# Optimization experiments

Measured on AMD Instinct MI355X. Metric: run time of the kernel, lower is better.

Reference implementation:

```python
import jax, jax.numpy as jnp
import numpy as np

B, V, K, D, E, NE = 32, 512, 16, 128, 32, 8192


def setup_inputs() -> dict:
    key = jax.random.key(0)
    ks = jax.random.split(key, 12)
    s = 0.05
    return {
        "vertex_features": jax.random.normal(ks[0], (B, V, D), jnp.float32),
        "atom_adj": jax.random.randint(ks[1], (B * V * K,), 0, B * V),
        "bond_adj": jax.random.randint(ks[2], (B * V * K,), 0, B * NE),
        "h0": jax.random.normal(ks[3], (B, V, D), jnp.float32),
        "lamda": jnp.full((1,), 0.5, jnp.float32),
        "alpha": jnp.full((1,), 0.1, jnp.float32),
        "l": 1,
        "edge_initial": jax.random.normal(ks[4], (B, NE, E), jnp.float32),
        "vertex_mask": jnp.ones((B, V), jnp.float32),
        "nbs_mask": jax.random.uniform(ks[5], (B, V, K), jnp.float32),
        # label_U1: (D+E) -> D ; label_U2: 2D -> D ; feature_updating: D -> D (variant=False)
        "W1": jax.random.normal(ks[6], (D, D + E), jnp.float32) * s,
        "b1": jax.random.normal(ks[7], (D,), jnp.float32) * s,
        "W2": jax.random.normal(ks[8], (D, 2 * D), jnp.float32) * s,
        "b2": jax.random.normal(ks[9], (D,), jnp.float32) * s,
        "W3": jax.random.normal(ks[10], (D, D), jnp.float32) * s,
        "b3": jax.random.normal(ks[11], (D,), jnp.float32) * s,
    }


def reference(vertex_features, atom_adj, bond_adj, h0, lamda, alpha, l,
              edge_initial, vertex_mask, nbs_mask, W1, b1, W2, b2, W3, b3):
    b, v = vertex_mask.shape
    k = nbs_mask.shape[2]
    d = vertex_features.shape[-1]
    e = edge_initial.shape[-1]
    # gather neighbor vertex and edge features (flat index, torch.index_select semantics)
    vn = vertex_features.reshape(-1, d)[atom_adj].reshape(b, v, k, d)
    en = edge_initial.reshape(-1, e)[bond_adj].reshape(b, v, k, e)
    l_neighbor = jnp.concatenate([vn, en], axis=-1)            # [b,v,k,d+e]
    nl = jax.nn.gelu(l_neighbor @ W1.T + b1, approximate=False)  # exact GELU like torch F.gelu
    nl = jnp.sum(nl * nbs_mask[..., None], axis=-2)            # masked sum over neighbors -> [b,v,d]
    hi = jnp.concatenate([nl, vertex_features], axis=-1) @ W2.T + b2
    theta = jnp.log(lamda / l + 1.0)                           # broadcast scalar (shape [1])
    support = (1.0 - alpha) * hi + alpha * h0                  # variant=False: r == support
    out = theta * (support @ W3.T + b3) + (1.0 - theta) * support
    out = out + vertex_features                                # residual=True
    return out
```

## Files before the change

### kernel.cpp

```cpp
#include <hip/hip_runtime.h>
#include <hip/hip_bf16.h>
#include <math.h>

#define NLSTR 136

typedef __bf16 bf16x8 __attribute__((ext_vector_type(8)));
typedef float f32x4 __attribute__((ext_vector_type(4)));
typedef unsigned short ushort8v __attribute__((ext_vector_type(8)));

union FragU { ushort8v u; bf16x8 b; };

static __device__ inline unsigned short f2bf(float f){
  unsigned u = __float_as_uint(f);
  u += 0x7fffu + ((u >> 16) & 1u);
  return (unsigned short)(u >> 16);
}

static __device__ inline float gelu_f(float x){
  float u = x * x;
  float p = fmaf(u, 0.07135481283f, 1.5957691216f);
  float t = x * p;
  float e = __builtin_amdgcn_exp2f(t * -1.44269504f);
  return x * __builtin_amdgcn_rcpf(1.0f + e);
}

__global__ __launch_bounds__(256) void prep_kernel(
    const float* __restrict__ vf, const float* __restrict__ W1,
    const float* __restrict__ W2, const float* __restrict__ W3,
    unsigned short* __restrict__ vfbf, unsigned short* __restrict__ w1f,
    unsigned short* __restrict__ w2f, unsigned short* __restrict__ w3f)
{
  int t = blockIdx.x * 256 + threadIdx.x;
  if (t < 262144){
    const float4* src = (const float4*)vf;
    float4 x = src[t * 2], y = src[t * 2 + 1];
    ushort8v o;
    o[0]=f2bf(x.x); o[1]=f2bf(x.y); o[2]=f2bf(x.z); o[3]=f2bf(x.w);
    o[4]=f2bf(y.x); o[5]=f2bf(y.y); o[6]=f2bf(y.z); o[7]=f2bf(y.w);
    *(ushort8v*)(vfbf + t * 8) = o;
    return;
  }
  int t2 = t - 262144;
  const float* W; unsigned short* O; int rowlen;
  if (t2 < 2560)      { W = W1; O = w1f; rowlen = 160; }
  else if (t2 < 6656) { t2 -= 2560; W = W2; O = w2f; rowlen = 256; }
  else if (t2 < 8704) { t2 -= 6656; W = W3; O = w3f; rowlen = 128; }
  else return;
  int fragid = t2 >> 6, lane = t2 & 63;
  int kc = fragid >> 3, nc = fragid & 7, col = lane & 15, quad = lane >> 4;
  const float* s = W + (nc * 16 + col) * rowlen + kc * 32 + quad * 8;
  unsigned short* d = O + t2 * 8;
#pragma unroll
  for (int j = 0; j < 8; j++) d[j] = f2bf(s[j]);
}

__global__ __launch_bounds__(256) void fused_kernel(
    const unsigned short* __restrict__ vfbf, const float* __restrict__ vf,
    const int* __restrict__ aadj, const int* __restrict__ badj,
    const float* __restrict__ edge, const float* __restrict__ nbs,
    const float* __restrict__ h0,
    const unsigned short* __restrict__ w1f, const unsigned short* __restrict__ w2f,
    const unsigned short* __restrict__ w3f,
    const float* __restrict__ b1, const float* __restrict__ b2, const float* __restrict__ b3,
    const float* __restrict__ lamda, const float* __restrict__ alpha,
    const int* __restrict__ lval,
    float* __restrict__ out)
{
  __shared__ __align__(16) unsigned short nl_lds[16 * NLSTR];
  __shared__ __align__(16) unsigned short sup_lds[16 * NLSTR];
  const int wid  = threadIdx.x >> 6;
  const int lane = threadIdx.x & 63;
  const int col  = lane & 15;
  const int quad = lane >> 4;
  const int v0   = blockIdx.x * 16;

  float b1v[8];
#pragma unroll
  for (int nc = 0; nc < 8; nc++) b1v[nc] = b1[nc * 16 + col];

  for (int it = 0; it < 4; ++it){
    const int vA = v0 + wid * 4 + it;
    const int a  = aadj[vA * 16 + col];
    const int e  = badj[vA * 16 + col];
    const float4 mk = ((const float4*)(nbs + vA * 16))[quad];

    FragU ef;
    {
      const float4* ep = (const float4*)(edge + (size_t)e * 32 + quad * 8);
      float4 xa = ep[0], xb = ep[1];
      ef.u[0]=f2bf(xa.x); ef.u[1]=f2bf(xa.y); ef.u[2]=f2bf(xa.z); ef.u[3]=f2bf(xa.w);
      ef.u[4]=f2bf(xb.x); ef.u[5]=f2bf(xb.y); ef.u[6]=f2bf(xb.z); ef.u[7]=f2bf(xb.w);
    }

    f32x4 acc[8] = {};
    const unsigned short* r = vfbf + (size_t)a * 128 + quad * 8;
#pragma unroll
    for (int kc = 0; kc < 4; kc++){
      FragU fa;
      fa.u = *(const ushort8v*)(r + kc * 32);
#pragma unroll
      for (int nc = 0; nc < 8; nc++){
        FragU bf_;
        bf_.u = *(const ushort8v*)(w1f + ((kc * 8 + nc) * 64 + lane) * 8);
        acc[nc] = __builtin_amdgcn_mfma_f32_16x16x32_bf16(fa.b, bf_.b, acc[nc], 0, 0, 0);
      }
    }
#pragma unroll
    for (int nc = 0; nc < 8; nc++){
      FragU bf_;
      bf_.u = *(const ushort8v*)(w1f + ((4 * 8 + nc) * 64 + lane) * 8);
      acc[nc] = __builtin_amdgcn_mfma_f32_16x16x32_bf16(ef.b, bf_.b, acc[nc], 0, 0, 0);
    }

    const int row = wid * 4 + it;
#pragma unroll
    for (int nc = 0; nc < 8; nc++){
      float g0 = gelu_f(acc[nc][0] + b1v[nc]);
      float g1 = gelu_f(acc[nc][1] + b1v[nc]);
      float g2 = gelu_f(acc[nc][2] + b1v[nc]);
      float g3 = gelu_f(acc[nc][3] + b1v[nc]);
      float s  = g0 * mk.x + g1 * mk.y + g2 * mk.z + g3 * mk.w;
      s += __shfl_xor(s, 16, 64);
      s += __shfl_xor(s, 32, 64);
      if ((nc >> 1) == quad)
        nl_lds[row * NLSTR + nc * 16 + col] = f2bf(s);
    }
  }
  __syncthreads();

  const int nc0 = 2 * wid;
  const float th = logf(lamda[0] / (float)lval[0] + 1.0f);
  const float al = alpha[0];

  f32x4 acc2[2] = {};
#pragma unroll
  for (int kc = 0; kc < 8; kc++){
    FragU a;
    if (kc < 4) a.u = *(const ushort8v*)(nl_lds + col * NLSTR + kc * 32 + quad * 8);
    else        a.u = *(const ushort8v*)(vfbf + (size_t)(v0 + col) * 128 + (kc - 4) * 32 + quad * 8);
#pragma unroll
    for (int p = 0; p < 2; p++){
      FragU bf_;
      bf_.u = *(const ushort8v*)(w2f + ((kc * 8 + nc0 + p) * 64 + lane) * 8);
      acc2[p] = __builtin_amdgcn_mfma_f32_16x16x32_bf16(a.b, bf_.b, acc2[p], 0, 0, 0);
    }
  }

  float sup[2][4];
#pragma unroll
  for (int p = 0; p < 2; p++){
    const int d = (nc0 + p) * 16 + col;
    const float bb = b2[d];
#pragma unroll
    for (int r = 0; r < 4; r++){
      const int vtx = v0 + quad * 4 + r;
      float hi = acc2[p][r] + bb;
      float s = (1.f - al) * hi + al * h0[vtx * 128 + d];
      sup[p][r] = s;
      sup_lds[(quad * 4 + r) * NLSTR + d] = f2bf(s);
    }
  }
  __syncthreads();

  f32x4 acc3[2] = {};
#pragma unroll
  for (int kc = 0; kc < 4; kc++){
    FragU a;
    a.u = *(const ushort8v*)(sup_lds + col * NLSTR + kc * 32 + quad * 8);
#pragma unroll
    for (int p = 0; p < 2; p++){
      FragU bf_;
      bf_.u = *(const ushort8v*)(w3f + ((kc * 8 + nc0 + p) * 64 + lane) * 8);
      acc3[p] = __builtin_amdgcn_mfma_f32_16x16x32_bf16(a.b, bf_.b, acc3[p], 0, 0, 0);
    }
  }

#pragma unroll
  for (int p = 0; p < 2; p++){
    const int d = (nc0 + p) * 16 + col;
    const float bb = b3[d];
#pragma unroll
    for (int r = 0; r < 4; r++){
      const int vtx = v0 + quad * 4 + r;
      out[vtx * 128 + d] = th * (acc3[p][r] + bb) + (1.f - th) * sup[p][r]
                         + vf[vtx * 128 + d];
    }
  }
}

extern "C" void kernel_launch(void* const* d_in, const int* in_sizes, int n_in,
                              void* d_out, int out_size, void* d_ws, size_t ws_size,
                              hipStream_t stream)
{
  const float* vfp  = (const float*)d_in[0];
  const int*   aadj = (const int*)d_in[1];
  const int*   badj = (const int*)d_in[2];
  const float* h0   = (const float*)d_in[3];
  const float* lam  = (const float*)d_in[4];
  const float* alp  = (const float*)d_in[5];
  const int*   lv   = (const int*)d_in[6];
  const float* edge = (const float*)d_in[7];
  const float* nbs  = (const float*)d_in[9];
  const float* W1   = (const float*)d_in[10];
  const float* b1   = (const float*)d_in[11];
  const float* W2   = (const float*)d_in[12];
  const float* b2   = (const float*)d_in[13];
  const float* W3   = (const float*)d_in[14];
  const float* b3   = (const float*)d_in[15];
  float* out = (float*)d_out;

  unsigned short* w1f  = (unsigned short*)d_ws;
  unsigned short* w2f  = w1f + 20480;
  unsigned short* w3f  = w2f + 32768;
  unsigned short* vfbf = w3f + 16384;

  prep_kernel<<<1058, 256, 0, stream>>>(vfp, W1, W2, W3, vfbf, w1f, w2f, w3f);
  fused_kernel<<<1024, 256, 0, stream>>>(vfbf, vfp, aadj, badj, edge, nbs, h0,
                                         w1f, w2f, w3f, b1, b2, b3, lam, alp, lv, out);
}
```

Baseline: 153.3 us.

## Switch first GEMM to 32x32x16 MFMA processing two vertices per wave

```diff
diff --git a/kernel.cpp b/kernel.cpp
--- a/kernel.cpp
+++ b/kernel.cpp
@@ -6,6 +6,7 @@
 
 typedef __bf16 bf16x8 __attribute__((ext_vector_type(8)));
 typedef float f32x4 __attribute__((ext_vector_type(4)));
+typedef float f32x16 __attribute__((ext_vector_type(16)));
 typedef unsigned short ushort8v __attribute__((ext_vector_type(8)));
 
 union FragU { ushort8v u; bf16x8 b; };
@@ -14,6 +15,9 @@
   unsigned u = __float_as_uint(f);
   u += 0x7fffu + ((u >> 16) & 1u);
   return (unsigned short)(u >> 16);
+}
+static __device__ inline float bf2f(unsigned short u){
+  return __uint_as_float(((unsigned)u) << 16);
 }
 
 static __device__ inline float gelu_f(float x){
@@ -41,21 +45,32 @@
     return;
   }
   int t2 = t - 262144;
-  const float* W; unsigned short* O; int rowlen;
-  if (t2 < 2560)      { W = W1; O = w1f; rowlen = 160; }
-  else if (t2 < 6656) { t2 -= 2560; W = W2; O = w2f; rowlen = 256; }
-  else if (t2 < 8704) { t2 -= 6656; W = W3; O = w3f; rowlen = 128; }
-  else return;
-  int fragid = t2 >> 6, lane = t2 & 63;
-  int kc = fragid >> 3, nc = fragid & 7, col = lane & 15, quad = lane >> 4;
-  const float* s = W + (nc * 16 + col) * rowlen + kc * 32 + quad * 8;
-  unsigned short* d = O + t2 * 8;
+  const float* s;
+  unsigned short* d;
+  if (t2 < 2560){
+    int fragid = t2 >> 6, lane = t2 & 63;
+    int kc = fragid >> 2, nc2 = fragid & 3, n = lane & 31, h = lane >> 5;
+    s = W1 + (nc2 * 32 + n) * 160 + kc * 16 + h * 8;
+    d = w1f + t2 * 8;
+  } else if (t2 < 6656){
+    int t3 = t2 - 2560;
+    int fragid = t3 >> 6, lane = t3 & 63;
+    int kc = fragid >> 3, nc = fragid & 7, col = lane & 15, quad = lane >> 4;
+    s = W2 + (nc * 16 + col) * 256 + kc * 32 + quad * 8;
+    d = w2f + t3 * 8;
+  } else if (t2 < 8704){
+    int t3 = t2 - 6656;
+    int fragid = t3 >> 6, lane = t3 & 63;
+    int kc = fragid >> 3, nc = fragid & 7, col = lane & 15, quad = lane >> 4;
+    s = W3 + (nc * 16 + col) * 128 + kc * 32 + quad * 8;
+    d = w3f + t3 * 8;
+  } else return;
 #pragma unroll
   for (int j = 0; j < 8; j++) d[j] = f2bf(s[j]);
 }
 
 __global__ __launch_bounds__(256) void fused_kernel(
-    const unsigned short* __restrict__ vfbf, const float* __restrict__ vf,
+    const unsigned short* __restrict__ vfbf,
     const int* __restrict__ aadj, const int* __restrict__ badj,
     const float* __restrict__ edge, const float* __restrict__ nbs,
     const float* __restrict__ h0,
@@ -70,60 +85,75 @@
   __shared__ __align__(16) unsigned short sup_lds[16 * NLSTR];
   const int wid  = threadIdx.x >> 6;
   const int lane = threadIdx.x & 63;
+  const int n32  = lane & 31;
+  const int h    = lane >> 5;
+  const int nb   = lane & 15;
+  const int vsel = (lane >> 4) & 1;
   const int col  = lane & 15;
   const int quad = lane >> 4;
   const int v0   = blockIdx.x * 16;
 
-  float b1v[8];
-#pragma unroll
-  for (int nc = 0; nc < 8; nc++) b1v[nc] = b1[nc * 16 + col];
-
-  for (int it = 0; it < 4; ++it){
-    const int vA = v0 + wid * 4 + it;
-    const int a  = aadj[vA * 16 + col];
-    const int e  = badj[vA * 16 + col];
-    const float4 mk = ((const float4*)(nbs + vA * 16))[quad];
-
-    FragU ef;
-    {
-      const float4* ep = (const float4*)(edge + (size_t)e * 32 + quad * 8);
-      float4 xa = ep[0], xb = ep[1];
-      ef.u[0]=f2bf(xa.x); ef.u[1]=f2bf(xa.y); ef.u[2]=f2bf(xa.z); ef.u[3]=f2bf(xa.w);
-      ef.u[4]=f2bf(xb.x); ef.u[5]=f2bf(xb.y); ef.u[6]=f2bf(xb.z); ef.u[7]=f2bf(xb.w);
-    }
-
-    f32x4 acc[8] = {};
-    const unsigned short* r = vfbf + (size_t)a * 128 + quad * 8;
-#pragma unroll
-    for (int kc = 0; kc < 4; kc++){
+  float b1v[4];
+#pragma unroll
+  for (int nc2 = 0; nc2 < 4; nc2++) b1v[nc2] = b1[nc2 * 32 + n32];
+
+  const ushort8v* w1v = (const ushort8v*)w1f;
+  const float4*   nbs4 = (const float4*)nbs;
+
+  for (int itp = 0; itp < 2; ++itp){
+    const int vA  = v0 + wid * 4 + itp * 2;
+    const int vtx = vA + vsel;
+    const int a = aadj[vtx * 16 + nb];
+    const int e = badj[vtx * 16 + nb];
+
+    ushort8v av[8];
+    const ushort8v* arow = (const ushort8v*)(vfbf + (size_t)a * 128 + h * 8);
+#pragma unroll
+    for (int kc = 0; kc < 8; kc++) av[kc] = arow[kc * 2];
+    float4 e0a = *(const float4*)(edge + (size_t)e * 32 + h * 8);
+    float4 e0b = *(const float4*)(edge + (size_t)e * 32 + h * 8 + 4);
+    float4 e1a = *(const float4*)(edge + (size_t)e * 32 + 16 + h * 8);
+    float4 e1b = *(const float4*)(edge + (size_t)e * 32 + 16 + h * 8 + 4);
+    const float4 mAlo = nbs4[vA * 4 + h],       mAhi = nbs4[vA * 4 + 2 + h];
+    const float4 mBlo = nbs4[(vA + 1) * 4 + h], mBhi = nbs4[(vA + 1) * 4 + 2 + h];
+
+    FragU ef[2];
+    ef[0].u[0]=f2bf(e0a.x); ef[0].u[1]=f2bf(e0a.y); ef[0].u[2]=f2bf(e0a.z); ef[0].u[3]=f2bf(e0a.w);
+    ef[0].u[4]=f2bf(e0b.x); ef[0].u[5]=f2bf(e0b.y); ef[0].u[6]=f2bf(e0b.z); ef[0].u[7]=f2bf(e0b.w);
+    ef[1].u[0]=f2bf(e1a.x); ef[1].u[1]=f2bf(e1a.y); ef[1].u[2]=f2bf(e1a.z); ef[1].u[3]=f2bf(e1a.w);
+    ef[1].u[4]=f2bf(e1b.x); ef[1].u[5]=f2bf(e1b.y); ef[1].u[6]=f2bf(e1b.z); ef[1].u[7]=f2bf(e1b.w);
+
+    f32x16 acc[4] = {};
+#pragma unroll
+    for (int kc = 0; kc < 10; kc++){
       FragU fa;
-      fa.u = *(const ushort8v*)(r + kc * 32);
-#pragma unroll
-      for (int nc = 0; nc < 8; nc++){
+      if (kc < 8) fa.u = av[kc];
+      else        fa.u = ef[kc - 8].u;
+#pragma unroll
+      for (int nc2 = 0; nc2 < 4; nc2++){
         FragU bf_;
-        bf_.u = *(const ushort8v*)(w1f + ((kc * 8 + nc) * 64 + lane) * 8);
-        acc[nc] = __builtin_amdgcn_mfma_f32_16x16x32_bf16(fa.b, bf_.b, acc[nc], 0, 0, 0);
+        bf_.u = w1v[(kc * 4 + nc2) * 64 + lane];
+        acc[nc2] = __builtin_amdgcn_mfma_f32_32x32x16_bf16(fa.b, bf_.b, acc[nc2], 0, 0, 0);
       }
     }
-#pragma unroll
-    for (int nc = 0; nc < 8; nc++){
-      FragU bf_;
-      bf_.u = *(const ushort8v*)(w1f + ((4 * 8 + nc) * 64 + lane) * 8);
-      acc[nc] = __builtin_amdgcn_mfma_f32_16x16x32_bf16(ef.b, bf_.b, acc[nc], 0, 0, 0);
-    }
-
-    const int row = wid * 4 + it;
-#pragma unroll
-    for (int nc = 0; nc < 8; nc++){
-      float g0 = gelu_f(acc[nc][0] + b1v[nc]);
-      float g1 = gelu_f(acc[nc][1] + b1v[nc]);
-      float g2 = gelu_f(acc[nc][2] + b1v[nc]);
-      float g3 = gelu_f(acc[nc][3] + b1v[nc]);
-      float s  = g0 * mk.x + g1 * mk.y + g2 * mk.z + g3 * mk.w;
-      s += __shfl_xor(s, 16, 64);
-      s += __shfl_xor(s, 32, 64);
-      if ((nc >> 1) == quad)
-        nl_lds[row * NLSTR + nc * 16 + col] = f2bf(s);
+
+    const int row = wid * 4 + itp * 2;
+#pragma unroll
+    for (int nc2 = 0; nc2 < 4; nc2++){
+      const float bb = b1v[nc2];
+      f32x16 ac = acc[nc2];
+      float sA = gelu_f(ac[0] + bb) * mAlo.x + gelu_f(ac[1] + bb) * mAlo.y
+               + gelu_f(ac[2] + bb) * mAlo.z + gelu_f(ac[3] + bb) * mAlo.w
+               + gelu_f(ac[4] + bb) * mAhi.x + gelu_f(ac[5] + bb) * mAhi.y
+               + gelu_f(ac[6] + bb) * mAhi.z + gelu_f(ac[7] + bb) * mAhi.w;
+      float sB = gelu_f(ac[8] + bb) * mBlo.x + gelu_f(ac[9] + bb) * mBlo.y
+               + gelu_f(ac[10] + bb) * mBlo.z + gelu_f(ac[11] + bb) * mBlo.w
+               + gelu_f(ac[12] + bb) * mBhi.x + gelu_f(ac[13] + bb) * mBhi.y
+               + gelu_f(ac[14] + bb) * mBhi.z + gelu_f(ac[15] + bb) * mBhi.w;
+      sA += __shfl_xor(sA, 32, 64);
+      sB += __shfl_xor(sB, 32, 64);
+      if (h == 0) nl_lds[row * NLSTR + nc2 * 32 + n32] = f2bf(sA);
+      else        nl_lds[(row + 1) * NLSTR + nc2 * 32 + n32] = f2bf(sB);
     }
   }
   __syncthreads();
@@ -182,8 +212,8 @@
 #pragma unroll
     for (int r = 0; r < 4; r++){
       const int vtx = v0 + quad * 4 + r;
-      out[vtx * 128 + d] = th * (acc3[p][r] + bb) + (1.f - th) * sup[p][r]
-                         + vf[vtx * 128 + d];
+      float res = bf2f(vfbf[(size_t)vtx * 128 + d]);
+      out[vtx * 128 + d] = th * (acc3[p][r] + bb) + (1.f - th) * sup[p][r] + res;
     }
   }
 }
@@ -215,6 +245,6 @@
   unsigned short* vfbf = w3f + 16384;
 
   prep_kernel<<<1058, 256, 0, stream>>>(vfp, W1, W2, W3, vfbf, w1f, w2f, w3f);
-  fused_kernel<<<1024, 256, 0, stream>>>(vfbf, vfp, aadj, badj, edge, nbs, h0,
+  fused_kernel<<<1024, 256, 0, stream>>>(vfbf, aadj, badj, edge, nbs, h0,
                                          w1f, w2f, w3f, b1, b2, b3, lam, alp, lv, out);
 }
```

Result: faster. 149.8 us (-2.2%).
